# Kernel tuning notes

Measured on AMD Instinct MI355X. Metric: run time of the kernel, lower is better.

Reference implementation:

```python
import jax, jax.numpy as jnp
import numpy as np

B, D, K = 4096, 768, 60


def setup_inputs() -> dict:
    key = jax.random.key(0)
    k1, k2, k3 = jax.random.split(key, 3)
    user_emb = jax.random.normal(k1, (B, D), dtype=jnp.float32)
    pos_item_emb = jax.random.normal(k2, (B, D), dtype=jnp.float32)
    # Per-row negative indices into the in-batch item table, excluding the
    # row's own positive (emulates the exclusion/sampling done on host in torch).
    r = jax.random.randint(k3, (B, K), 0, B, dtype=jnp.int32)
    rows = jnp.arange(B, dtype=jnp.int32)[:, None]
    neg_indices = jnp.where(r == rows, (r + 1) % B, r)
    return {"user_emb": user_emb, "pos_item_emb": pos_item_emb,
            "neg_indices": neg_indices}


def reference(user_emb, pos_item_emb, neg_indices):
    # u2i contrastive loss: logits = [u.pos, u.neg_1..neg_K], label 0, mean CE.
    logits_pos = jnp.sum(user_emb * pos_item_emb, axis=-1)          # (B,)
    neg_embs = pos_item_emb[neg_indices]                            # (B, K, D)
    logits_neg = jnp.einsum('bd,bkd->bk', user_emb, neg_embs)      # (B, K)
    logits = jnp.concatenate([logits_pos[:, None], logits_neg], axis=1)
    loss = -jax.nn.log_softmax(logits, axis=-1)[:, 0]               # label = 0
    return jnp.mean(loss)
```

## Files before the change

kernel.cpp:

```cpp
#include <hip/hip_runtime.h>
#include <hip/hip_bf16.h>
#include <hip/hip_fp16.h>
#include <math.h>


#define NB 4096
#define ND 768
#define NK 60
#define ND4  (ND / 4)
#define NDU  (ND / 2)
#define NLOGITS (NK + 1)
#define NPAD 64

#define WS_LOGITS_OFF 0
#define WS_ITEMS_OFF  ((size_t)NB * NPAD * 4)
#define WS_LOSS_OFF   (WS_ITEMS_OFF + (size_t)NB * ND * 2)
#define WS_NEED       (WS_LOSS_OFF + (size_t)NB * 4)

typedef _Float16 h2 __attribute__((ext_vector_type(2)));
typedef float    f2 __attribute__((ext_vector_type(2)));

__device__ __forceinline__ float dot2_acc(unsigned int u, unsigned int v, float c) {
#if __has_builtin(__builtin_amdgcn_fdot2)
    return __builtin_amdgcn_fdot2(__builtin_bit_cast(h2, u),
                                  __builtin_bit_cast(h2, v), c, false);
#else
    f2 a = __builtin_convertvector(__builtin_bit_cast(h2, u), f2);
    f2 b = __builtin_convertvector(__builtin_bit_cast(h2, v), f2);
    return c + a.x * b.x + a.y * b.y;
#endif
}

__device__ __forceinline__ unsigned int pack_h2(float x, float y) {
    h2 h = { (_Float16)x, (_Float16)y };
    return __builtin_bit_cast(unsigned int, h);
}

__global__ __launch_bounds__(256) void convert_items_f16(
    const float4* __restrict__ items, uint2* __restrict__ itemsh)
{
    int i = blockIdx.x * 256 + threadIdx.x;
    float4 v = items[i];
    uint2 rv;
    rv.x = pack_h2(v.x, v.y);
    rv.y = pack_h2(v.z, v.w);
    itemsh[i] = rv;
}

__global__ __launch_bounds__(256, 4) void gather_dots(
    const float* __restrict__ user,
    const unsigned int* __restrict__ itemsh,
    const int* __restrict__ negidx,
    float* __restrict__ logits)
{
    const int tid  = threadIdx.x;
    const int lane = tid & 63;
    const int w    = blockIdx.x * 4 + (tid >> 6);
    const int b    = w >> 3;
    const int slot = w & 7;

    const int* nrow = negidx + (size_t)b * NK;
    int rows[8];
    #pragma unroll
    for (int i = 0; i < 8; ++i) {
        int k = slot * 8 + i;
        rows[i] = (k == 0 || k > NK) ? b : nrow[k - 1];
    }

    const float4* ur4 = (const float4*)(user + (size_t)b * ND);
    float4 uf0 = ur4[2 * lane];
    float4 uf1 = ur4[2 * lane + 1];
    float4 uf2 = ur4[128 + lane];
    uint4 ua;
    ua.x = pack_h2(uf0.x, uf0.y);
    ua.y = pack_h2(uf0.z, uf0.w);
    ua.z = pack_h2(uf1.x, uf1.y);
    ua.w = pack_h2(uf1.z, uf1.w);
    uint2 ub;
    ub.x = pack_h2(uf2.x, uf2.y);
    ub.y = pack_h2(uf2.z, uf2.w);

    uint4 va[8];
    uint2 vb[8];
    #pragma unroll
    for (int i = 0; i < 8; ++i) {
        const unsigned int* ir = itemsh + (size_t)rows[i] * NDU;
        va[i] = ((const uint4*)ir)[lane];
        vb[i] = ((const uint2*)(ir + 256))[lane];
    }

    float acc[8];
    #pragma unroll
    for (int i = 0; i < 8; ++i) {
        float a = 0.0f;
        a = dot2_acc(ua.x, va[i].x, a);
        a = dot2_acc(ua.y, va[i].y, a);
        a = dot2_acc(ua.z, va[i].z, a);
        a = dot2_acc(ua.w, va[i].w, a);
        a = dot2_acc(ub.x, vb[i].x, a);
        a = dot2_acc(ub.y, vb[i].y, a);
        acc[i] = a;
    }

    const int bit0 = lane & 1;
    float n[4];
    #pragma unroll
    for (int j = 0; j < 4; ++j) {
        float mine  = bit0 ? acc[2*j+1] : acc[2*j];
        float other = bit0 ? acc[2*j]   : acc[2*j+1];
        n[j] = mine + __shfl_xor(other, 1, 64);
    }
    const int bit1 = (lane >> 1) & 1;
    float s[2];
    #pragma unroll
    for (int j = 0; j < 2; ++j) {
        float mine  = bit1 ? n[2*j+1] : n[2*j];
        float other = bit1 ? n[2*j]   : n[2*j+1];
        s[j] = mine + __shfl_xor(other, 2, 64);
    }
    const int bit2 = (lane >> 2) & 1;
    {
        float mine  = bit2 ? s[1] : s[0];
        float other = bit2 ? s[0] : s[1];
        float r = mine + __shfl_xor(other, 4, 64);
        r += __shfl_xor(r, 8, 64);
        r += __shfl_xor(r, 16, 64);
        r += __shfl_xor(r, 32, 64);
        if (lane < 8)
            logits[(size_t)b * NPAD + slot * 8 + lane] = r;
    }
}

__global__ __launch_bounds__(256) void lse_loss(
    const float* __restrict__ logits, float* __restrict__ loss)
{
    const int tid  = threadIdx.x;
    const int lane = tid & 63;
    const int b    = blockIdx.x * 4 + (tid >> 6);

    float v  = (lane < NLOGITS) ? logits[(size_t)b * NPAD + lane] : -INFINITY;
    float p0 = __shfl(v, 0, 64);
    float m = v;
    #pragma unroll
    for (int off = 32; off > 0; off >>= 1)
        m = fmaxf(m, __shfl_down(m, off, 64));
    m = __shfl(m, 0, 64);
    float e = (lane < NLOGITS) ? __expf(v - m) : 0.0f;
    #pragma unroll
    for (int off = 32; off > 0; off >>= 1)
        e += __shfl_down(e, off, 64);
    if (lane == 0)
        loss[b] = m + __logf(e) - p0;
}

__global__ __launch_bounds__(256) void final_reduce(
    const float* __restrict__ loss, float* __restrict__ out)
{
    const int tid = threadIdx.x;
    const float4* l4 = (const float4*)loss;
    float s = 0.0f;
    #pragma unroll
    for (int j = 0; j < 4; ++j) {
        float4 v = l4[tid + 256 * j];
        s += v.x + v.y + v.z + v.w;
    }
    #pragma unroll
    for (int off = 32; off > 0; off >>= 1)
        s += __shfl_down(s, off, 64);
    __shared__ float ps[4];
    if ((tid & 63) == 0) ps[tid >> 6] = s;
    __syncthreads();
    if (tid == 0)
        out[0] = (ps[0] + ps[1] + ps[2] + ps[3]) * (1.0f / (float)NB);
}

__global__ __launch_bounds__(256) void u2i_loss_f32(
    const float* __restrict__ user,
    const float* __restrict__ items,
    const int* __restrict__ negidx,
    float* __restrict__ out)
{
    const int b    = blockIdx.x;
    const int tid  = threadIdx.x;
    const int wave = tid >> 6;
    const int lane = tid & 63;

    __shared__ int   rows_s[NPAD];
    __shared__ float logits[NPAD];

    if (tid < NPAD) {
        const int* nrow = negidx + (size_t)b * NK;
        rows_s[tid] = (tid == 0 || tid > NK) ? b : nrow[tid - 1];
    }
    const float4* u4 = (const float4*)user + (size_t)b * ND4;
    float4 u0 = u4[lane];
    float4 u1 = u4[64 + lane];
    float4 u2 = u4[128 + lane];
    __syncthreads();

    const float4* it4 = (const float4*)items;
    #pragma unroll
    for (int j = 0; j < 4; ++j) {
        int ks[4];
        const float4* p[4];
        #pragma unroll
        for (int i = 0; i < 4; ++i) {
            ks[i] = wave + j * 16 + i * 4;
            p[i]  = it4 + (size_t)rows_s[ks[i]] * ND4;
        }
        float4 v0[4], v1[4], v2[4];
        #pragma unroll
        for (int i = 0; i < 4; ++i) {
            v0[i] = p[i][lane];
            v1[i] = p[i][64 + lane];
            v2[i] = p[i][128 + lane];
        }
        float acc[4];
        #pragma unroll
        for (int i = 0; i < 4; ++i) {
            float a;
            a  = u0.x * v0[i].x + u0.y * v0[i].y + u0.z * v0[i].z + u0.w * v0[i].w;
            a += u1.x * v1[i].x + u1.y * v1[i].y + u1.z * v1[i].z + u1.w * v1[i].w;
            a += u2.x * v2[i].x + u2.y * v2[i].y + u2.z * v2[i].z + u2.w * v2[i].w;
            acc[i] = a;
        }
        #pragma unroll
        for (int off = 32; off > 0; off >>= 1) {
            #pragma unroll
            for (int i = 0; i < 4; ++i)
                acc[i] += __shfl_down(acc[i], off, 64);
        }
        if (lane == 0) {
            #pragma unroll
            for (int i = 0; i < 4; ++i)
                logits[ks[i]] = acc[i];
        }
    }
    __syncthreads();

    if (tid < 64) {
        float v = (tid < NLOGITS) ? logits[tid] : -INFINITY;
        float m = v;
        #pragma unroll
        for (int off = 32; off > 0; off >>= 1)
            m = fmaxf(m, __shfl_down(m, off, 64));
        m = __shfl(m, 0, 64);
        float e = (tid < NLOGITS) ? __expf(v - m) : 0.0f;
        #pragma unroll
        for (int off = 32; off > 0; off >>= 1)
            e += __shfl_down(e, off, 64);
        if (tid == 0) {
            float loss = m + __logf(e) - logits[0];
            atomicAdd(out, loss * (1.0f / (float)NB));
        }
    }
}

extern "C" void kernel_launch(void* const* d_in, const int* in_sizes, int n_in,
                              void* d_out, int out_size, void* d_ws, size_t ws_size,
                              hipStream_t stream) {
    const float* user  = (const float*)d_in[0];
    const float* items = (const float*)d_in[1];
    const int*   negi  = (const int*)d_in[2];
    float* out = (float*)d_out;

    if (ws_size >= WS_NEED) {
        char* ws = (char*)d_ws;
        float* logits = (float*)(ws + WS_LOGITS_OFF);
        uint2* itemsh = (uint2*)(ws + WS_ITEMS_OFF);
        float* loss   = (float*)(ws + WS_LOSS_OFF);

        convert_items_f16<<<(NB * ND / 4) / 256, 256, 0, stream>>>(
            (const float4*)items, itemsh);
        gather_dots<<<NB * 8 / 4, 256, 0, stream>>>(
            user, (const unsigned int*)itemsh, negi, logits);
        lse_loss<<<NB / 4, 256, 0, stream>>>(logits, loss);
        final_reduce<<<1, 256, 0, stream>>>(loss, out);
    } else {
        hipMemsetAsync(out, 0, sizeof(float), stream);
        u2i_loss_f32<<<NB, 256, 0, stream>>>(user, items, negi, out);
    }
}
```

Measured before the change: 103.4 us.

## Split f16 item table into two dimension planes and fuse LSE into second pass

Converts items into two separate f16 planes (first 512 dims and last 256 dims) and performs the gather dot products in two passes, so each pass gathers from a smaller table that is more likely to stay cache-resident. The second pass adds the partial logits from the first and computes the log-sum-exp loss in the same kernel, removing the separate lse kernel. This costs a second round of index and user-row loads and an extra partial-logit write/read.

```diff
diff --git a/kernel.cpp b/kernel.cpp
--- a/kernel.cpp
+++ b/kernel.cpp
@@ -8,13 +8,16 @@
 #define ND 768
 #define NK 60
 #define ND4  (ND / 4)
-#define NDU  (ND / 2)
 #define NLOGITS (NK + 1)
 #define NPAD 64
 
-#define WS_LOGITS_OFF 0
-#define WS_ITEMS_OFF  ((size_t)NB * NPAD * 4)
-#define WS_LOSS_OFF   (WS_ITEMS_OFF + (size_t)NB * ND * 2)
+#define PA_ROW_U 256
+#define PB_ROW_U 128
+
+#define WS_LOGP_OFF   0
+#define WS_PLANEA_OFF ((size_t)NB * NPAD * 4)
+#define WS_PLANEB_OFF (WS_PLANEA_OFF + (size_t)NB * PA_ROW_U * 4)
+#define WS_LOSS_OFF   (WS_PLANEB_OFF + (size_t)NB * PB_ROW_U * 4)
 #define WS_NEED       (WS_LOSS_OFF + (size_t)NB * 4)
 
 typedef _Float16 h2 __attribute__((ext_vector_type(2)));
@@ -36,22 +39,58 @@
     return __builtin_bit_cast(unsigned int, h);
 }
 
-__global__ __launch_bounds__(256) void convert_items_f16(
-    const float4* __restrict__ items, uint2* __restrict__ itemsh)
-{
-    int i = blockIdx.x * 256 + threadIdx.x;
+__device__ __forceinline__ float fold8(const float acc[8], int lane) {
+    const int bit0 = lane & 1;
+    float n[4];
+    #pragma unroll
+    for (int j = 0; j < 4; ++j) {
+        float mine  = bit0 ? acc[2*j+1] : acc[2*j];
+        float other = bit0 ? acc[2*j]   : acc[2*j+1];
+        n[j] = mine + __shfl_xor(other, 1, 64);
+    }
+    const int bit1 = (lane >> 1) & 1;
+    float s[2];
+    #pragma unroll
+    for (int j = 0; j < 2; ++j) {
+        float mine  = bit1 ? s[0] * 0.0f + (bit1 ? n[2*j+1] : n[2*j]) : n[2*j];
+        (void)mine;
+        float mm = bit1 ? n[2*j+1] : n[2*j];
+        float other = bit1 ? n[2*j] : n[2*j+1];
+        s[j] = mm + __shfl_xor(other, 2, 64);
+    }
+    const int bit2 = (lane >> 2) & 1;
+    float mine2  = bit2 ? s[1] : s[0];
+    float other2 = bit2 ? s[0] : s[1];
+    float r = mine2 + __shfl_xor(other2, 4, 64);
+    r += __shfl_xor(r, 8, 64);
+    r += __shfl_xor(r, 16, 64);
+    r += __shfl_xor(r, 32, 64);
+    return r;
+}
+
+__global__ __launch_bounds__(256) void convert_items_planes(
+    const float4* __restrict__ items,
+    unsigned int* __restrict__ planeA,
+    unsigned int* __restrict__ planeB)
+{
+    int i  = blockIdx.x * 256 + threadIdx.x;
+    int b  = i / ND4;
+    int d4 = i - b * ND4;
     float4 v = items[i];
     uint2 rv;
     rv.x = pack_h2(v.x, v.y);
     rv.y = pack_h2(v.z, v.w);
-    itemsh[i] = rv;
-}
-
-__global__ __launch_bounds__(256, 4) void gather_dots(
+    if (d4 < 128)
+        ((uint2*)planeA)[(size_t)b * 128 + d4] = rv;
+    else
+        ((uint2*)planeB)[(size_t)b * 64 + (d4 - 128)] = rv;
+}
+
+__global__ __launch_bounds__(256, 4) void gather_dots_a(
     const float* __restrict__ user,
-    const unsigned int* __restrict__ itemsh,
+    const unsigned int* __restrict__ planeA,
     const int* __restrict__ negidx,
-    float* __restrict__ logits)
+    float* __restrict__ logp)
 {
     const int tid  = threadIdx.x;
     const int lane = tid & 63;
@@ -70,24 +109,16 @@
     const float4* ur4 = (const float4*)(user + (size_t)b * ND);
     float4 uf0 = ur4[2 * lane];
     float4 uf1 = ur4[2 * lane + 1];
-    float4 uf2 = ur4[128 + lane];
     uint4 ua;
     ua.x = pack_h2(uf0.x, uf0.y);
     ua.y = pack_h2(uf0.z, uf0.w);
     ua.z = pack_h2(uf1.x, uf1.y);
     ua.w = pack_h2(uf1.z, uf1.w);
-    uint2 ub;
-    ub.x = pack_h2(uf2.x, uf2.y);
-    ub.y = pack_h2(uf2.z, uf2.w);
 
     uint4 va[8];
-    uint2 vb[8];
-    #pragma unroll
-    for (int i = 0; i < 8; ++i) {
-        const unsigned int* ir = itemsh + (size_t)rows[i] * NDU;
-        va[i] = ((const uint4*)ir)[lane];
-        vb[i] = ((const uint2*)(ir + 256))[lane];
-    }
+    #pragma unroll
+    for (int i = 0; i < 8; ++i)
+        va[i] = ((const uint4*)(planeA + (size_t)rows[i] * PA_ROW_U))[lane];
 
     float acc[8];
     #pragma unroll
@@ -97,60 +128,77 @@
         a = dot2_acc(ua.y, va[i].y, a);
         a = dot2_acc(ua.z, va[i].z, a);
         a = dot2_acc(ua.w, va[i].w, a);
+        acc[i] = a;
+    }
+
+    float r = fold8(acc, lane);
+    if (lane < 8)
+        logp[(size_t)b * NPAD + slot * 8 + lane] = r;
+}
+
+__global__ __launch_bounds__(512, 4) void gather_dots_b_lse(
+    const float* __restrict__ user,
+    const unsigned int* __restrict__ planeB,
+    const int* __restrict__ negidx,
+    const float* __restrict__ logp,
+    float* __restrict__ loss)
+{
+    const int tid  = threadIdx.x;
+    const int lane = tid & 63;
+    const int slot = tid >> 6;
+    const int b    = blockIdx.x;
+
+    const int* nrow = negidx + (size_t)b * NK;
+    int rows[8];
+    #pragma unroll
+    for (int i = 0; i < 8; ++i) {
+        int k = slot * 8 + i;
+        rows[i] = (k == 0 || k > NK) ? b : nrow[k - 1];
+    }
+
+    const float4* ur4 = (const float4*)(user + (size_t)b * ND);
+    float4 uf2 = ur4[128 + lane];
+    uint2 ub;
+    ub.x = pack_h2(uf2.x, uf2.y);
+    ub.y = pack_h2(uf2.z, uf2.w);
+
+    uint2 vb[8];
+    #pragma unroll
+    for (int i = 0; i < 8; ++i)
+        vb[i] = ((const uint2*)(planeB + (size_t)rows[i] * PB_ROW_U))[lane];
+
+    float acc[8];
+    #pragma unroll
+    for (int i = 0; i < 8; ++i) {
+        float a = 0.0f;
         a = dot2_acc(ub.x, vb[i].x, a);
         a = dot2_acc(ub.y, vb[i].y, a);
         acc[i] = a;
     }
 
-    const int bit0 = lane & 1;
-    float n[4];
-    #pragma unroll
-    for (int j = 0; j < 4; ++j) {
-        float mine  = bit0 ? acc[2*j+1] : acc[2*j];
-        float other = bit0 ? acc[2*j]   : acc[2*j+1];
-        n[j] = mine + __shfl_xor(other, 1, 64);
-    }
-    const int bit1 = (lane >> 1) & 1;
-    float s[2];
-    #pragma unroll
-    for (int j = 0; j < 2; ++j) {
-        float mine  = bit1 ? n[2*j+1] : n[2*j];
-        float other = bit1 ? n[2*j]   : n[2*j+1];
-        s[j] = mine + __shfl_xor(other, 2, 64);
-    }
-    const int bit2 = (lane >> 2) & 1;
-    {
-        float mine  = bit2 ? s[1] : s[0];
-        float other = bit2 ? s[0] : s[1];
-        float r = mine + __shfl_xor(other, 4, 64);
-        r += __shfl_xor(r, 8, 64);
-        r += __shfl_xor(r, 16, 64);
-        r += __shfl_xor(r, 32, 64);
-        if (lane < 8)
-            logits[(size_t)b * NPAD + slot * 8 + lane] = r;
-    }
-}
-
-__global__ __launch_bounds__(256) void lse_loss(
-    const float* __restrict__ logits, float* __restrict__ loss)
-{
-    const int tid  = threadIdx.x;
-    const int lane = tid & 63;
-    const int b    = blockIdx.x * 4 + (tid >> 6);
-
-    float v  = (lane < NLOGITS) ? logits[(size_t)b * NPAD + lane] : -INFINITY;
-    float p0 = __shfl(v, 0, 64);
-    float m = v;
-    #pragma unroll
-    for (int off = 32; off > 0; off >>= 1)
-        m = fmaxf(m, __shfl_down(m, off, 64));
-    m = __shfl(m, 0, 64);
-    float e = (lane < NLOGITS) ? __expf(v - m) : 0.0f;
-    #pragma unroll
-    for (int off = 32; off > 0; off >>= 1)
-        e += __shfl_down(e, off, 64);
-    if (lane == 0)
-        loss[b] = m + __logf(e) - p0;
+    float r = fold8(acc, lane);
+
+    __shared__ float lg[NPAD];
+    float part = logp[(size_t)b * NPAD + slot * 8 + (lane & 7)];
+    if (lane < 8)
+        lg[slot * 8 + lane] = r + part;
+    __syncthreads();
+
+    if (tid < 64) {
+        float v  = (tid < NLOGITS) ? lg[tid] : -INFINITY;
+        float p0 = lg[0];
+        float m = v;
+        #pragma unroll
+        for (int off = 32; off > 0; off >>= 1)
+            m = fmaxf(m, __shfl_down(m, off, 64));
+        m = __shfl(m, 0, 64);
+        float e = (tid < NLOGITS) ? __expf(v - m) : 0.0f;
+        #pragma unroll
+        for (int off = 32; off > 0; off >>= 1)
+            e += __shfl_down(e, off, 64);
+        if (tid == 0)
+            loss[b] = m + __logf(e) - p0;
+    }
 }
 
 __global__ __launch_bounds__(256) void final_reduce(
@@ -266,15 +314,17 @@
 
     if (ws_size >= WS_NEED) {
         char* ws = (char*)d_ws;
-        float* logits = (float*)(ws + WS_LOGITS_OFF);
-        uint2* itemsh = (uint2*)(ws + WS_ITEMS_OFF);
-        float* loss   = (float*)(ws + WS_LOSS_OFF);
-
-        convert_items_f16<<<(NB * ND / 4) / 256, 256, 0, stream>>>(
-            (const float4*)items, itemsh);
-        gather_dots<<<NB * 8 / 4, 256, 0, stream>>>(
-            user, (const unsigned int*)itemsh, negi, logits);
-        lse_loss<<<NB / 4, 256, 0, stream>>>(logits, loss);
+        float*        logp   = (float*)(ws + WS_LOGP_OFF);
+        unsigned int* planeA = (unsigned int*)(ws + WS_PLANEA_OFF);
+        unsigned int* planeB = (unsigned int*)(ws + WS_PLANEB_OFF);
+        float*        loss   = (float*)(ws + WS_LOSS_OFF);
+
+        convert_items_planes<<<(NB * ND / 4) / 256, 256, 0, stream>>>(
+            (const float4*)items, planeA, planeB);
+        gather_dots_a<<<NB * 8 / 4, 256, 0, stream>>>(
+            user, planeA, negi, logp);
+        gather_dots_b_lse<<<NB, 512, 0, stream>>>(
+            user, planeB, negi, logp, loss);
         final_reduce<<<1, 256, 0, stream>>>(loss, out);
     } else {
         hipMemsetAsync(out, 0, sizeof(float), stream);
```

Result: no change. 104.7 us (+1.2%).

## Fuse gather-dot, log-sum-exp and mean into one kernel per batch row

Applied to the files above, without the earlier changes.

Merges the gather/dot kernel, the per-row LSE kernel and the final reduction into a single 512-thread block per row. Logits are exchanged through shared memory and the mean is built with an atomicAdd, so the logits and loss workspace round trips and two kernel launches go away. The fp32 item read in the conversion kernel becomes a nontemporal load. In exchange there are 4096 atomics on one address, a memset launch on the fast path, and a non-deterministic summation order.

```diff
diff --git a/kernel.cpp b/kernel.cpp
--- a/kernel.cpp
+++ b/kernel.cpp
@@ -12,13 +12,12 @@
 #define NLOGITS (NK + 1)
 #define NPAD 64
 
-#define WS_LOGITS_OFF 0
-#define WS_ITEMS_OFF  ((size_t)NB * NPAD * 4)
-#define WS_LOSS_OFF   (WS_ITEMS_OFF + (size_t)NB * ND * 2)
-#define WS_NEED       (WS_LOSS_OFF + (size_t)NB * 4)
+#define WS_ITEMS_OFF 0
+#define WS_NEED      ((size_t)NB * ND * 2)
 
 typedef _Float16 h2 __attribute__((ext_vector_type(2)));
 typedef float    f2 __attribute__((ext_vector_type(2)));
+typedef float    f4v __attribute__((ext_vector_type(4)));
 
 __device__ __forceinline__ float dot2_acc(unsigned int u, unsigned int v, float c) {
 #if __has_builtin(__builtin_amdgcn_fdot2)
@@ -36,28 +35,54 @@
     return __builtin_bit_cast(unsigned int, h);
 }
 
+__device__ __forceinline__ float fold8(const float acc[8], int lane) {
+    const int bit0 = lane & 1;
+    float n[4];
+    #pragma unroll
+    for (int j = 0; j < 4; ++j) {
+        float mine  = bit0 ? acc[2*j+1] : acc[2*j];
+        float other = bit0 ? acc[2*j]   : acc[2*j+1];
+        n[j] = mine + __shfl_xor(other, 1, 64);
+    }
+    const int bit1 = (lane >> 1) & 1;
+    float s[2];
+    #pragma unroll
+    for (int j = 0; j < 2; ++j) {
+        float mine  = bit1 ? n[2*j+1] : n[2*j];
+        float other = bit1 ? n[2*j]   : n[2*j+1];
+        s[j] = mine + __shfl_xor(other, 2, 64);
+    }
+    const int bit2 = (lane >> 2) & 1;
+    float mine  = bit2 ? s[1] : s[0];
+    float other = bit2 ? s[0] : s[1];
+    float r = mine + __shfl_xor(other, 4, 64);
+    r += __shfl_xor(r, 8, 64);
+    r += __shfl_xor(r, 16, 64);
+    r += __shfl_xor(r, 32, 64);
+    return r;
+}
+
 __global__ __launch_bounds__(256) void convert_items_f16(
-    const float4* __restrict__ items, uint2* __restrict__ itemsh)
+    const f4v* __restrict__ items, uint2* __restrict__ itemsh)
 {
     int i = blockIdx.x * 256 + threadIdx.x;
-    float4 v = items[i];
+    f4v v = __builtin_nontemporal_load(items + i);
     uint2 rv;
     rv.x = pack_h2(v.x, v.y);
     rv.y = pack_h2(v.z, v.w);
     itemsh[i] = rv;
 }
 
-__global__ __launch_bounds__(256, 4) void gather_dots(
+__global__ __launch_bounds__(512, 4) void fused_gather_lse(
     const float* __restrict__ user,
     const unsigned int* __restrict__ itemsh,
     const int* __restrict__ negidx,
-    float* __restrict__ logits)
+    float* __restrict__ out)
 {
     const int tid  = threadIdx.x;
     const int lane = tid & 63;
-    const int w    = blockIdx.x * 4 + (tid >> 6);
-    const int b    = w >> 3;
-    const int slot = w & 7;
+    const int slot = tid >> 6;
+    const int b    = blockIdx.x;
 
     const int* nrow = negidx + (size_t)b * NK;
     int rows[8];
@@ -102,76 +127,30 @@
         acc[i] = a;
     }
 
-    const int bit0 = lane & 1;
-    float n[4];
-    #pragma unroll
-    for (int j = 0; j < 4; ++j) {
-        float mine  = bit0 ? acc[2*j+1] : acc[2*j];
-        float other = bit0 ? acc[2*j]   : acc[2*j+1];
-        n[j] = mine + __shfl_xor(other, 1, 64);
-    }
-    const int bit1 = (lane >> 1) & 1;
-    float s[2];
-    #pragma unroll
-    for (int j = 0; j < 2; ++j) {
-        float mine  = bit1 ? n[2*j+1] : n[2*j];
-        float other = bit1 ? n[2*j]   : n[2*j+1];
-        s[j] = mine + __shfl_xor(other, 2, 64);
-    }
-    const int bit2 = (lane >> 2) & 1;
-    {
-        float mine  = bit2 ? s[1] : s[0];
-        float other = bit2 ? s[0] : s[1];
-        float r = mine + __shfl_xor(other, 4, 64);
-        r += __shfl_xor(r, 8, 64);
-        r += __shfl_xor(r, 16, 64);
-        r += __shfl_xor(r, 32, 64);
-        if (lane < 8)
-            logits[(size_t)b * NPAD + slot * 8 + lane] = r;
-    }
-}
-
-__global__ __launch_bounds__(256) void lse_loss(
-    const float* __restrict__ logits, float* __restrict__ loss)
-{
-    const int tid  = threadIdx.x;
-    const int lane = tid & 63;
-    const int b    = blockIdx.x * 4 + (tid >> 6);
-
-    float v  = (lane < NLOGITS) ? logits[(size_t)b * NPAD + lane] : -INFINITY;
-    float p0 = __shfl(v, 0, 64);
-    float m = v;
-    #pragma unroll
-    for (int off = 32; off > 0; off >>= 1)
-        m = fmaxf(m, __shfl_down(m, off, 64));
-    m = __shfl(m, 0, 64);
-    float e = (lane < NLOGITS) ? __expf(v - m) : 0.0f;
-    #pragma unroll
-    for (int off = 32; off > 0; off >>= 1)
-        e += __shfl_down(e, off, 64);
-    if (lane == 0)
-        loss[b] = m + __logf(e) - p0;
-}
-
-__global__ __launch_bounds__(256) void final_reduce(
-    const float* __restrict__ loss, float* __restrict__ out)
-{
-    const int tid = threadIdx.x;
-    const float4* l4 = (const float4*)loss;
-    float s = 0.0f;
-    #pragma unroll
-    for (int j = 0; j < 4; ++j) {
-        float4 v = l4[tid + 256 * j];
-        s += v.x + v.y + v.z + v.w;
-    }
-    #pragma unroll
-    for (int off = 32; off > 0; off >>= 1)
-        s += __shfl_down(s, off, 64);
-    __shared__ float ps[4];
-    if ((tid & 63) == 0) ps[tid >> 6] = s;
+    float r = fold8(acc, lane);
+
+    __shared__ float lg[NPAD];
+    if (lane < 8)
+        lg[slot * 8 + lane] = r;
     __syncthreads();
-    if (tid == 0)
-        out[0] = (ps[0] + ps[1] + ps[2] + ps[3]) * (1.0f / (float)NB);
+
+    if (tid < 64) {
+        float v  = (tid < NLOGITS) ? lg[tid] : -INFINITY;
+        float p0 = lg[0];
+        float m = v;
+        #pragma unroll
+        for (int off = 32; off > 0; off >>= 1)
+            m = fmaxf(m, __shfl_down(m, off, 64));
+        m = __shfl(m, 0, 64);
+        float e = (tid < NLOGITS) ? __expf(v - m) : 0.0f;
+        #pragma unroll
+        for (int off = 32; off > 0; off >>= 1)
+            e += __shfl_down(e, off, 64);
+        if (tid == 0) {
+            float loss = m + __logf(e) - p0;
+            atomicAdd(out, loss * (1.0f / (float)NB));
+        }
+    }
 }
 
 __global__ __launch_bounds__(256) void u2i_loss_f32(
@@ -264,20 +243,16 @@
     const int*   negi  = (const int*)d_in[2];
     float* out = (float*)d_out;
 
+    hipMemsetAsync(out, 0, sizeof(float), stream);
+
     if (ws_size >= WS_NEED) {
-        char* ws = (char*)d_ws;
-        float* logits = (float*)(ws + WS_LOGITS_OFF);
-        uint2* itemsh = (uint2*)(ws + WS_ITEMS_OFF);
-        float* loss   = (float*)(ws + WS_LOSS_OFF);
+        unsigned int* itemsh = (unsigned int*)((char*)d_ws + WS_ITEMS_OFF);
 
         convert_items_f16<<<(NB * ND / 4) / 256, 256, 0, stream>>>(
-            (const float4*)items, itemsh);
-        gather_dots<<<NB * 8 / 4, 256, 0, stream>>>(
-            user, (const unsigned int*)itemsh, negi, logits);
-        lse_loss<<<NB / 4, 256, 0, stream>>>(logits, loss);
-        final_reduce<<<1, 256, 0, stream>>>(loss, out);
+            (const f4v*)items, (uint2*)itemsh);
+        fused_gather_lse<<<NB, 512, 0, stream>>>(
+            user, itemsh, negi, out);
     } else {
-        hipMemsetAsync(out, 0, sizeof(float), stream);
         u2i_loss_f32<<<NB, 256, 0, stream>>>(user, items, negi, out);
     }
 }
```

Result: slower. 134.8 us (+30.3%).
